# Performance work log

Hardware: AMD Instinct MI355X
Metric: run time of the kernel (lower is better)

## Reference

```python
import jax, jax.numpy as jnp
import numpy as np
from jax import lax

N_LAYER = 4
D_MODEL = 1024
D_INNER = 2048   # expand=2
D_STATE = 16
DT_RANK = 64     # ceil(d_model/16)
D_CONV = 4
BATCH = 2
SEQ = 2048
EPS = 1e-5


def setup_inputs() -> dict:
    key = jax.random.key(0)
    ks = jax.random.split(key, 8)
    rn = lambda k, shape, s=0.02: jax.random.normal(k, shape, dtype=jnp.float32) * s
    # S4D-real init for A_log, as in mamba_ssm
    A_init = jnp.tile(jnp.arange(1, D_STATE + 1, dtype=jnp.float32)[None, None, :],
                      (N_LAYER, D_INNER, 1))
    return {
        "hidden_states": jax.random.normal(ks[0], (BATCH, SEQ, D_MODEL), dtype=jnp.float32),
        "norm_w": jnp.ones((N_LAYER, D_MODEL), jnp.float32),
        "norm_b": jnp.zeros((N_LAYER, D_MODEL), jnp.float32),
        "in_proj_w": rn(ks[1], (N_LAYER, 2 * D_INNER, D_MODEL)),
        "conv_w": rn(ks[2], (N_LAYER, D_INNER, D_CONV), 0.1),
        "conv_b": jnp.zeros((N_LAYER, D_INNER), jnp.float32),
        "x_proj_w": rn(ks[3], (N_LAYER, DT_RANK + 2 * D_STATE, D_INNER)),
        "dt_proj_w": rn(ks[4], (N_LAYER, D_INNER, DT_RANK), 0.1),
        "dt_proj_b": rn(ks[5], (N_LAYER, D_INNER), 0.1),
        "A_log": jnp.log(A_init),
        "D": jnp.ones((N_LAYER, D_INNER), jnp.float32),
        "out_proj_w": rn(ks[6], (N_LAYER, D_MODEL, D_INNER)),
        "final_norm_w": jnp.ones((D_MODEL,), jnp.float32),
        "final_norm_b": jnp.zeros((D_MODEL,), jnp.float32),
    }


def _layernorm(x, w, b):
    mu = jnp.mean(x, axis=-1, keepdims=True)
    var = jnp.mean(jnp.square(x - mu), axis=-1, keepdims=True)
    return (x - mu) * lax.rsqrt(var + EPS) * w + b


def _mamba_block(h, in_w, conv_w, conv_b, x_w, dt_w, dt_b, A_log, Dp, out_w):
    B, L, _ = h.shape
    xz = jnp.einsum('bld,ed->ble', h, in_w)               # [B,L,2*d_inner]
    x, z = jnp.split(xz, 2, axis=-1)
    # depthwise causal conv1d (kernel D_CONV), truncated to L
    xp = jnp.pad(x, ((0, 0), (D_CONV - 1, 0), (0, 0)))
    x = sum(xp[:, k:k + L, :] * conv_w[:, k] for k in range(D_CONV)) + conv_b
    x = jax.nn.silu(x)
    x_dbl = jnp.einsum('bld,ed->ble', x, x_w)             # [B,L,dt_rank+2*d_state]
    dt, Bm, Cm = jnp.split(x_dbl, [DT_RANK, DT_RANK + D_STATE], axis=-1)
    delta = jax.nn.softplus(jnp.einsum('blr,dr->bld', dt, dt_w) + dt_b)  # [B,L,d_inner]
    A = -jnp.exp(A_log)                                   # [d_inner, d_state]

    def step(state, xs):
        d_t, B_t, C_t, u_t = xs                           # [B,di],[B,ds],[B,ds],[B,di]
        dA = jnp.exp(d_t[..., None] * A)                  # [B,di,ds]
        state = dA * state + (d_t * u_t)[..., None] * B_t[:, None, :]
        y_t = jnp.einsum('bds,bs->bd', state, C_t)
        return state, y_t

    xs = (jnp.swapaxes(delta, 0, 1), jnp.swapaxes(Bm, 0, 1),
          jnp.swapaxes(Cm, 0, 1), jnp.swapaxes(x, 0, 1))
    init = jnp.zeros((B, D_INNER, D_STATE), dtype=h.dtype)
    _, ys = lax.scan(step, init, xs)                      # ys: [L,B,di]
    y = jnp.swapaxes(ys, 0, 1) + x * Dp
    y = y * jax.nn.silu(z)
    return jnp.einsum('bld,ed->ble', y, out_w)            # [B,L,d_model]


def reference(hidden_states, norm_w, norm_b, in_proj_w, conv_w, conv_b,
              x_proj_w, dt_proj_w, dt_proj_b, A_log, D, out_proj_w,
              final_norm_w, final_norm_b):
    residual = None
    for i in range(N_LAYER):
        residual = hidden_states + residual if residual is not None else hidden_states
        h = _layernorm(residual, norm_w[i], norm_b[i])
        hidden_states = _mamba_block(h, in_proj_w[i], conv_w[i], conv_b[i],
                                     x_proj_w[i], dt_proj_w[i], dt_proj_b[i],
                                     A_log[i], D[i], out_proj_w[i])
    residual = hidden_states + residual
    return _layernorm(residual, final_norm_w, final_norm_b)
```

## Files before the change

kernel.cpp:

```cpp
#include <hip/hip_runtime.h>
#include <math.h>

#define N_LAYERS 4
#define DMODEL 1024
#define DINNER 2048
#define DSTATE 16
#define DTRANK 64
#define DCONV 4
#define NBATCH 2
#define LSEQ 2048
#define LNEPS 1e-5f
#define ROWS (NBATCH * LSEQ)
#define CLEN 16
#define NCHUNK (LSEQ / CLEN)
#define XP 128
#define KSLICE 512
#define NSLICE (DINNER / KSLICE)

typedef __attribute__((ext_vector_type(8))) short bf16x8;
typedef __attribute__((ext_vector_type(8))) unsigned short ushort8;
typedef __attribute__((ext_vector_type(4))) float f32x4;

__device__ __forceinline__ unsigned short f2bf(float f) {
  unsigned int u = __float_as_uint(f);
  return (unsigned short)((u + 0x7FFFu + ((u >> 16) & 1u)) >> 16);
}
__device__ __forceinline__ float bf2f(unsigned short h) {
  return __uint_as_float(((unsigned int)h) << 16);
}

__device__ __forceinline__ void gload16(const unsigned short* g, unsigned short* l) {
  __builtin_amdgcn_global_load_lds(
      (const __attribute__((address_space(1))) unsigned int*)g,
      (__attribute__((address_space(3))) unsigned int*)l, 16, 0, 0);
}

__device__ __forceinline__ float softplus_f(float x) {
  float e = __expf(-fabsf(x));
  return fmaxf(x, 0.f) + __logf(1.f + e);
}

__global__ __launch_bounds__(256) void cvt_f2bf(const float* __restrict__ src,
                                                unsigned short* __restrict__ dst, int n4) {
  int i = blockIdx.x * 256 + threadIdx.x;
  if (i >= n4) return;
  float4 v = ((const float4*)src)[i];
  ushort4 o;
  o.x = f2bf(v.x); o.y = f2bf(v.y); o.z = f2bf(v.z); o.w = f2bf(v.w);
  ((ushort4*)dst)[i] = o;
}

__global__ __launch_bounds__(256) void cvt_xpw(const float* __restrict__ src,
                                               unsigned short* __restrict__ dst) {
  int i = blockIdx.x * 256 + threadIdx.x;
  int col4 = i & 511;
  int row = (i >> 9) & 127;
  int layer = i >> 16;
  float4 v = make_float4(0.f, 0.f, 0.f, 0.f);
  if (row < 96) v = ((const float4*)(src + ((size_t)layer * 96 + row) * 2048))[col4];
  ushort4 o;
  o.x = f2bf(v.x); o.y = f2bf(v.y); o.z = f2bf(v.z); o.w = f2bf(v.w);
  ((ushort4*)(dst + ((size_t)layer * 128 + row) * 2048))[col4] = o;
}

template<bool OBF>
__global__ __launch_bounds__(256) void ln_kernel(
    const float* __restrict__ src, float* __restrict__ res_copy,
    const float* __restrict__ w, const float* __restrict__ b, void* out) {
  int row = blockIdx.x;
  int t = threadIdx.x;
  const float4* srow = (const float4*)(src + (size_t)row * DMODEL);
  float4 v = srow[t];
  if (res_copy) ((float4*)(res_copy + (size_t)row * DMODEL))[t] = v;
  float s = v.x + v.y + v.z + v.w;
  float sq = v.x * v.x + v.y * v.y + v.z * v.z + v.w * v.w;
  #pragma unroll
  for (int o = 32; o >= 1; o >>= 1) {
    s += __shfl_xor(s, o);
    sq += __shfl_xor(sq, o);
  }
  __shared__ float ss[4], ssq[4];
  int wid = t >> 6, lane = t & 63;
  if (lane == 0) { ss[wid] = s; ssq[wid] = sq; }
  __syncthreads();
  s = ss[0] + ss[1] + ss[2] + ss[3];
  sq = ssq[0] + ssq[1] + ssq[2] + ssq[3];
  float mu = s * (1.f / DMODEL);
  float var = sq * (1.f / DMODEL) - mu * mu;
  float rs = rsqrtf(var + LNEPS);
  float4 wv = ((const float4*)w)[t];
  float4 bv = ((const float4*)b)[t];
  float4 o4;
  o4.x = (v.x - mu) * rs * wv.x + bv.x;
  o4.y = (v.y - mu) * rs * wv.y + bv.y;
  o4.z = (v.z - mu) * rs * wv.z + bv.z;
  o4.w = (v.w - mu) * rs * wv.w + bv.w;
  if (OBF) {
    ushort4 ob;
    ob.x = f2bf(o4.x); ob.y = f2bf(o4.y); ob.z = f2bf(o4.z); ob.w = f2bf(o4.w);
    ((ushort4*)((unsigned short*)out + (size_t)row * DMODEL))[t] = ob;
  } else {
    ((float4*)((float*)out + (size_t)row * DMODEL))[t] = o4;
  }
}

template<int ACT, bool BIAS, bool ADD, bool WF32, bool WBF>
__global__ __launch_bounds__(512) void gemm256(
    const unsigned short* __restrict__ A, int lda,
    const unsigned short* __restrict__ W, int ldw,
    float* __restrict__ C, int ldc, int K,
    const float* __restrict__ bias,
    const float* __restrict__ addsrc,
    unsigned short* __restrict__ Cb) {
  __shared__ unsigned short lds[2][2][256][64];
  const int t = threadIdx.x;
  const int lane = t & 63;
  const int wave = t >> 6;
  const int wr = wave >> 2;
  const int wc = wave & 3;
  const int m0 = blockIdx.y * 256, n0 = blockIdx.x * 256;

  const int srow = t >> 3;
  const int sslot = t & 7;
  const int frow = lane & 15;
  const int hi = lane >> 4;

  f32x4 acc[8][4];
  #pragma unroll
  for (int m = 0; m < 8; m++)
    #pragma unroll
    for (int n = 0; n < 4; n++) acc[m][n] = (f32x4){0.f, 0.f, 0.f, 0.f};

  const int NT = K / 64;

  auto stage = [&](int buf, int kt) {
    const int scol = (sslot << 3) + kt * 64;
    #pragma unroll
    for (int r = 0; r < 4; ++r) {
      int row = srow + (r << 6);
      gload16(A + (size_t)(m0 + row) * lda + scol, &lds[buf][0][row][sslot << 3]);
    }
    #pragma unroll
    for (int r = 0; r < 4; ++r) {
      int row = srow + (r << 6);
      gload16(W + (size_t)(n0 + row) * ldw + scol, &lds[buf][1][row][sslot << 3]);
    }
  };

  auto compute = [&](int buf) {
    #pragma unroll
    for (int ks = 0; ks < 2; ++ks) {
      bf16x8 a[8], b[4];
      #pragma unroll
      for (int m = 0; m < 8; ++m) {
        int row = wr * 128 + m * 16 + frow;
        a[m] = *(const bf16x8*)&lds[buf][0][row][(ks * 4 + hi) << 3];
      }
      #pragma unroll
      for (int n = 0; n < 4; ++n) {
        int row = wc * 64 + n * 16 + frow;
        b[n] = *(const bf16x8*)&lds[buf][1][row][(ks * 4 + hi) << 3];
      }
      __builtin_amdgcn_s_setprio(1);
      #pragma unroll
      for (int m = 0; m < 8; ++m)
        #pragma unroll
        for (int n = 0; n < 4; ++n)
          acc[m][n] = __builtin_amdgcn_mfma_f32_16x16x32_bf16(a[m], b[n], acc[m][n], 0, 0, 0);
      __builtin_amdgcn_s_setprio(0);
    }
  };

  stage(0, 0);
  if (NT > 1) stage(1, 1);
  for (int kt = 0; kt < NT - 1; ++kt) {
    asm volatile("s_waitcnt vmcnt(8)" ::: "memory");
    __builtin_amdgcn_s_barrier();
    asm volatile("" ::: "memory");
    compute(kt & 1);
    __builtin_amdgcn_s_barrier();
    asm volatile("" ::: "memory");
    if (kt + 2 < NT) stage(kt & 1, kt + 2);
  }
  asm volatile("s_waitcnt vmcnt(0)" ::: "memory");
  __builtin_amdgcn_s_barrier();
  asm volatile("" ::: "memory");
  compute((NT - 1) & 1);

  #pragma unroll
  for (int m = 0; m < 8; ++m) {
    int rbase = m0 + wr * 128 + m * 16 + hi * 4;
    #pragma unroll
    for (int n = 0; n < 4; ++n) {
      int ccol = n0 + wc * 64 + n * 16 + frow;
      #pragma unroll
      for (int j = 0; j < 4; ++j) {
        int crow = rbase + j;
        float v = acc[m][n][j];
        if (BIAS) v += bias[ccol];
        if (ACT == 1) v = softplus_f(v);
        if (ADD) v += addsrc[(size_t)crow * ldc + ccol];
        if (WF32) C[(size_t)crow * ldc + ccol] = v;
        if (WBF) Cb[(size_t)crow * ldc + ccol] = f2bf(v);
      }
    }
  }
}

template<int ACT, bool BIAS, bool ADD, bool WF32, bool WBF, bool PARTIAL>
__global__ __launch_bounds__(256) void gemm_bf16(
    const unsigned short* __restrict__ A, int lda,
    const unsigned short* __restrict__ W, int ldw,
    float* __restrict__ C, int ldc, int K,
    const float* __restrict__ bias,
    const float* __restrict__ addsrc,
    unsigned short* __restrict__ Cb) {
  __shared__ unsigned short As[2][128][32];
  __shared__ unsigned short Ws[2][128][32];
  int t = threadIdx.x;
  int lane = t & 63, wave = t >> 6;
  int wr = wave >> 1, wc = wave & 1;
  int m0 = blockIdx.y * 128, n0 = blockIdx.x * 128;

  int kbase = 0;
  if (PARTIAL) {
    kbase = blockIdx.z * K;
    C += (size_t)blockIdx.z * (size_t)gridDim.y * 128 * ldc;
  }

  int r0 = t >> 2;
  int kk8 = (t & 3) << 3;
  const unsigned short* Ag = A + (size_t)(m0 + r0) * lda + kbase + kk8;
  const unsigned short* Wg = W + (size_t)(n0 + r0) * ldw + kbase + kk8;
  const size_t Astep = (size_t)64 * lda;
  const size_t Wstep = (size_t)64 * ldw;

  f32x4 zero = {0.f, 0.f, 0.f, 0.f};
  f32x4 acc[4][4];
  #pragma unroll
  for (int m = 0; m < 4; m++)
    #pragma unroll
    for (int n = 0; n < 4; n++) acc[m][n] = zero;

  int frow = lane & 15;
  int fk = (lane >> 4) << 3;

  auto stage = [&](int buf, int kt) {
    const unsigned short* ag = Ag + kt * 32;
    const unsigned short* wg = Wg + kt * 32;
    unsigned short* la = &As[buf][r0][kk8];
    unsigned short* lw = &Ws[buf][r0][kk8];
    gload16(ag, la);
    gload16(ag + Astep, la + 64 * 32);
    gload16(wg, lw);
    gload16(wg + Wstep, lw + 64 * 32);
  };
  auto compute = [&](int buf) {
    bf16x8 af[4], bw[4];
    #pragma unroll
    for (int m = 0; m < 4; m++)
      af[m] = *(const bf16x8*)&As[buf][wr * 64 + m * 16 + frow][fk];
    #pragma unroll
    for (int n = 0; n < 4; n++)
      bw[n] = *(const bf16x8*)&Ws[buf][wc * 64 + n * 16 + frow][fk];
    #pragma unroll
    for (int m = 0; m < 4; m++)
      #pragma unroll
      for (int n = 0; n < 4; n++)
        acc[m][n] = __builtin_amdgcn_mfma_f32_16x16x32_bf16(af[m], bw[n], acc[m][n], 0, 0, 0);
  };

  const int NT = K / 32;
  stage(0, 0);
  __syncthreads();
  int cur = 0;
  for (int kt = 0; kt < NT - 1; ++kt) {
    stage(cur ^ 1, kt + 1);
    compute(cur);
    __syncthreads();
    cur ^= 1;
  }
  compute(cur);

  #pragma unroll
  for (int m = 0; m < 4; m++) {
    int rbase = m0 + wr * 64 + m * 16 + ((lane >> 4) << 2);
    #pragma unroll
    for (int n = 0; n < 4; n++) {
      int ccol = n0 + wc * 64 + n * 16 + (lane & 15);
      #pragma unroll
      for (int j = 0; j < 4; j++) {
        int crow = rbase + j;
        float v = acc[m][n][j];
        if (BIAS) v += bias[ccol];
        if (ACT == 1) v = softplus_f(v);
        if (ADD) v += addsrc[(size_t)crow * ldc + ccol];
        if (WF32 || PARTIAL) C[(size_t)crow * ldc + ccol] = v;
        if (WBF) Cb[(size_t)crow * ldc + ccol] = f2bf(v);
      }
    }
  }
}

__global__ __launch_bounds__(256) void combine_xdbl(
    const float* __restrict__ part, float* __restrict__ xdbl,
    unsigned short* __restrict__ xdbl_bf) {
  int i = blockIdx.x * 256 + threadIdx.x;
  const size_t slab = (size_t)ROWS * XP / 4;
  const float4* p = (const float4*)part;
  float4 a = p[i], b = p[i + slab], c = p[i + 2 * slab], d = p[i + 3 * slab];
  float4 s;
  s.x = a.x + b.x + c.x + d.x;
  s.y = a.y + b.y + c.y + d.y;
  s.z = a.z + b.z + c.z + d.z;
  s.w = a.w + b.w + c.w + d.w;
  ((float4*)xdbl)[i] = s;
  ushort4 o;
  o.x = f2bf(s.x); o.y = f2bf(s.y); o.z = f2bf(s.z); o.w = f2bf(s.w);
  ((ushort4*)xdbl_bf)[i] = o;
}

__global__ __launch_bounds__(256) void conv_silu_kernel(
    const unsigned short* __restrict__ xz, const float* __restrict__ cw,
    const float* __restrict__ cb, unsigned short* __restrict__ xbf) {
  int tid = blockIdx.x * 256 + threadIdx.x;
  int dv = tid & (DINNER / 8 - 1);
  int rg = tid >> 8;
  int l0 = (rg & (LSEQ / 4 - 1)) * 4;
  int row0 = rg * 4;
  int d = dv * 8;

  float4 wq[8];
  #pragma unroll
  for (int j = 0; j < 8; j++) wq[j] = ((const float4*)(cw + (size_t)d * DCONV))[j];
  float4 b0 = ((const float4*)(cb + d))[0];
  float4 b1 = ((const float4*)(cb + d))[1];
  const float bias[8] = {b0.x, b0.y, b0.z, b0.w, b1.x, b1.y, b1.z, b1.w};

  ushort8 xin[7];
  #pragma unroll
  for (int r = 0; r < 7; r++) {
    int l = l0 - 3 + r;
    if (l >= 0)
      xin[r] = *(const ushort8*)(xz + (size_t)(row0 - 3 + r) * (2 * DINNER) + d);
    else
      xin[r] = (ushort8){0, 0, 0, 0, 0, 0, 0, 0};
  }

  #pragma unroll
  for (int o = 0; o < 4; o++) {
    ushort8 ob;
    #pragma unroll
    for (int j = 0; j < 8; j++) {
      const float* wj = (const float*)&wq[j];
      float acc = bias[j];
      #pragma unroll
      for (int k = 0; k < DCONV; k++)
        acc = fmaf(bf2f(xin[o + k][j]), wj[k], acc);
      float s = acc / (1.f + __expf(-acc));
      ob[j] = f2bf(s);
    }
    *(ushort8*)(xbf + (size_t)(row0 + o) * DINNER + d) = ob;
  }
}

__global__ __launch_bounds__(256) void scan_p1(
    const float* __restrict__ delta, const unsigned short* __restrict__ u,
    const float* __restrict__ xdbl, const float* __restrict__ A_log,
    float* __restrict__ aprodbuf, float* __restrict__ statebuf) {
  int tid = blockIdx.x * 256 + threadIdx.x;
  int t = threadIdx.x;
  int d = tid & (DINNER - 1);
  int chunk = (tid >> 11) & (NCHUNK - 1);
  int b = tid >> 18;
  int l0 = chunk * CLEN;

  __shared__ float bl[CLEN][16];
  {
    const float4* src4 = (const float4*)(xdbl + ((size_t)b * LSEQ + l0) * XP);
    if (t < CLEN * 4) {
      int li = t >> 2, qi = t & 3;
      ((float4*)&bl[li][0])[qi] = src4[li * (XP / 4) + 16 + qi];
    }
  }
  __syncthreads();

  float A[DSTATE], st[DSTATE], ap[DSTATE];
  const float4* Ar = (const float4*)(A_log + d * DSTATE);
  #pragma unroll
  for (int q = 0; q < 4; q++) {
    float4 av = Ar[q];
    A[4 * q] = -__expf(av.x); A[4 * q + 1] = -__expf(av.y);
    A[4 * q + 2] = -__expf(av.z); A[4 * q + 3] = -__expf(av.w);
  }
  #pragma unroll
  for (int s = 0; s < DSTATE; s++) { st[s] = 0.f; ap[s] = 1.f; }

  const float* dptr = delta + ((size_t)b * LSEQ + l0) * DINNER + d;
  const unsigned short* uptr = u + ((size_t)b * LSEQ + l0) * DINNER + d;
  float dt_n = dptr[0];
  float uu_n = bf2f(uptr[0]);
  #pragma unroll
  for (int l = 0; l < CLEN; l++) {
    float dt = dt_n, uu = uu_n;
    if (l + 1 < CLEN) {
      dt_n = dptr[(size_t)(l + 1) * DINNER];
      uu_n = bf2f(uptr[(size_t)(l + 1) * DINNER]);
    }
    float du = dt * uu;
    #pragma unroll
    for (int q = 0; q < 4; q++) {
      float4 B4 = *(const float4*)&bl[l][q * 4];
      const float Bj[4] = {B4.x, B4.y, B4.z, B4.w};
      #pragma unroll
      for (int j = 0; j < 4; j++) {
        int s = 4 * q + j;
        float dA = __expf(dt * A[s]);
        st[s] = fmaf(dA, st[s], du * Bj[j]);
        ap[s] *= dA;
      }
    }
  }
  float4* apo = (float4*)(aprodbuf + (size_t)tid * DSTATE);
  float4* sto = (float4*)(statebuf + (size_t)tid * DSTATE);
  #pragma unroll
  for (int q = 0; q < 4; q++) {
    apo[q] = make_float4(ap[4 * q], ap[4 * q + 1], ap[4 * q + 2], ap[4 * q + 3]);
    sto[q] = make_float4(st[4 * q], st[4 * q + 1], st[4 * q + 2], st[4 * q + 3]);
  }
}

__global__ __launch_bounds__(256) void scan_p2(
    float* apc, const float* __restrict__ statebuf) {
  int tid = blockIdx.x * 256 + threadIdx.x;
  int ds = tid & (DINNER * DSTATE - 1);
  int b = tid >> 15;
  float carry = 0.f;
  size_t base = (size_t)b * NCHUNK * DINNER * DSTATE + ds;
  const size_t cs = DINNER * DSTATE;
  for (int c = 0; c < NCHUNK; c += 4) {
    size_t i0 = base + (size_t)c * cs;
    float a0 = apc[i0], a1 = apc[i0 + cs], a2 = apc[i0 + 2 * cs], a3 = apc[i0 + 3 * cs];
    float s0 = statebuf[i0], s1 = statebuf[i0 + cs];
    float s2 = statebuf[i0 + 2 * cs], s3 = statebuf[i0 + 3 * cs];
    apc[i0] = carry;          carry = fmaf(a0, carry, s0);
    apc[i0 + cs] = carry;     carry = fmaf(a1, carry, s1);
    apc[i0 + 2 * cs] = carry; carry = fmaf(a2, carry, s2);
    apc[i0 + 3 * cs] = carry; carry = fmaf(a3, carry, s3);
  }
}

__global__ __launch_bounds__(256) void scan_p3(
    const float* __restrict__ delta, const unsigned short* __restrict__ u,
    const float* __restrict__ xdbl, const unsigned short* __restrict__ xzbf,
    const float* __restrict__ A_log, const float* __restrict__ Dp,
    const float* __restrict__ carryin, unsigned short* __restrict__ ybf) {
  int tid = blockIdx.x * 256 + threadIdx.x;
  int t = threadIdx.x;
  int d = tid & (DINNER - 1);
  int chunk = (tid >> 11) & (NCHUNK - 1);
  int b = tid >> 18;
  int l0 = chunk * CLEN;

  __shared__ float bc[CLEN][32];
  {
    const float4* src4 = (const float4*)(xdbl + ((size_t)b * LSEQ + l0) * XP);
    if (t < CLEN * 8) {
      int li = t >> 3, qi = t & 7;
      ((float4*)&bc[li][0])[qi] = src4[li * (XP / 4) + 16 + qi];
    }
  }
  __syncthreads();

  float A[DSTATE], st[DSTATE];
  const float4* ci = (const float4*)(carryin + (size_t)tid * DSTATE);
  #pragma unroll
  for (int q = 0; q < 4; q++) {
    float4 cv = ci[q];
    st[4 * q] = cv.x; st[4 * q + 1] = cv.y; st[4 * q + 2] = cv.z; st[4 * q + 3] = cv.w;
  }
  const float4* Ar = (const float4*)(A_log + d * DSTATE);
  #pragma unroll
  for (int q = 0; q < 4; q++) {
    float4 av = Ar[q];
    A[4 * q] = -__expf(av.x); A[4 * q + 1] = -__expf(av.y);
    A[4 * q + 2] = -__expf(av.z); A[4 * q + 3] = -__expf(av.w);
  }
  float Dval = Dp[d];

  const float* dptr = delta + ((size_t)b * LSEQ + l0) * DINNER + d;
  const unsigned short* uptr = u + ((size_t)b * LSEQ + l0) * DINNER + d;
  const unsigned short* zptr = xzbf + ((size_t)b * LSEQ + l0) * (2 * DINNER) + DINNER + d;
  unsigned short* yptr = ybf + ((size_t)b * LSEQ + l0) * DINNER + d;

  float dt_n = dptr[0];
  float uu_n = bf2f(uptr[0]);
  float zz_n = bf2f(zptr[0]);
  #pragma unroll
  for (int l = 0; l < CLEN; l++) {
    float dt = dt_n, uu = uu_n, zz = zz_n;
    if (l + 1 < CLEN) {
      dt_n = dptr[(size_t)(l + 1) * DINNER];
      uu_n = bf2f(uptr[(size_t)(l + 1) * DINNER]);
      zz_n = bf2f(zptr[(size_t)(l + 1) * (2 * DINNER)]);
    }
    float du = dt * uu;
    #pragma unroll
    for (int q = 0; q < 4; q++) {
      float4 B4 = *(const float4*)&bc[l][q * 4];
      const float Bj[4] = {B4.x, B4.y, B4.z, B4.w};
      #pragma unroll
      for (int j = 0; j < 4; j++) {
        int s = 4 * q + j;
        float dA = __expf(dt * A[s]);
        st[s] = fmaf(dA, st[s], du * Bj[j]);
      }
    }
    float acc = 0.f;
    #pragma unroll
    for (int q = 0; q < 4; q++) {
      float4 C4 = *(const float4*)&bc[l][16 + q * 4];
      const float Cj[4] = {C4.x, C4.y, C4.z, C4.w};
      #pragma unroll
      for (int j = 0; j < 4; j++) acc = fmaf(st[4 * q + j], Cj[j], acc);
    }
    float yv = (acc + uu * Dval) * (zz / (1.f + __expf(-zz)));
    yptr[(size_t)l * DINNER] = f2bf(yv);
  }
}

extern "C" void kernel_launch(void* const* d_in, const int* in_sizes, int n_in,
                              void* d_out, int out_size, void* d_ws, size_t ws_size,
                              hipStream_t stream) {
  const float* hidden    = (const float*)d_in[0];
  const float* norm_w    = (const float*)d_in[1];
  const float* norm_b    = (const float*)d_in[2];
  const float* in_proj_w = (const float*)d_in[3];
  const float* conv_w    = (const float*)d_in[4];
  const float* conv_b    = (const float*)d_in[5];
  const float* x_proj_w  = (const float*)d_in[6];
  const float* dt_proj_w = (const float*)d_in[7];
  const float* dt_proj_b = (const float*)d_in[8];
  const float* A_log     = (const float*)d_in[9];
  const float* Dp        = (const float*)d_in[10];
  const float* out_proj_w= (const float*)d_in[11];
  const float* fnw       = (const float*)d_in[12];
  const float* fnb       = (const float*)d_in[13];
  float* out = (float*)d_out;

  const size_t CARRYSZ = (size_t)NBATCH * NCHUNK * DINNER * DSTATE;

  float* residual = (float*)d_ws;
  float* delta    = residual + (size_t)ROWS * DMODEL;
  float* aprod    = delta + (size_t)ROWS * DINNER;
  float* statebuf = aprod + CARRYSZ;
  float* xdbl     = statebuf + CARRYSZ;
  float* fend     = xdbl + (size_t)ROWS * XP;

  unsigned short* xz_bf   = (unsigned short*)fend;
  unsigned short* xbuf_bf = xz_bf + (size_t)ROWS * 2 * DINNER;
  unsigned short* xdbl_bf = xbuf_bf + (size_t)ROWS * DINNER;
  unsigned short* xpw_bf  = xdbl_bf + (size_t)ROWS * XP;
  unsigned short* dtw_bf  = xpw_bf + (size_t)N_LAYERS * XP * DINNER;
  unsigned short* ipw_bf  = dtw_bf + (size_t)N_LAYERS * DINNER * DTRANK;
  unsigned short* opw_bf  = ipw_bf + (size_t)2 * DINNER * DMODEL;

  unsigned short* h_bf    = (unsigned short*)statebuf;
  unsigned short* ybuf_bf = (unsigned short*)statebuf;
  float*          carryin = aprod;
  float*          xpart   = delta;

  cvt_xpw<<<N_LAYERS * XP * DINNER / 4 / 256, 256, 0, stream>>>(x_proj_w, xpw_bf);
  {
    int n4 = N_LAYERS * DINNER * DTRANK / 4;
    cvt_f2bf<<<n4 / 256, 256, 0, stream>>>(dt_proj_w, dtw_bf, n4);
  }

  for (int i = 0; i < N_LAYERS; i++) {
    {
      int n4 = 2 * DINNER * DMODEL / 4;
      cvt_f2bf<<<n4 / 256, 256, 0, stream>>>(
          in_proj_w + (size_t)i * 2 * DINNER * DMODEL, ipw_bf, n4);
      n4 = DMODEL * DINNER / 4;
      cvt_f2bf<<<n4 / 256, 256, 0, stream>>>(
          out_proj_w + (size_t)i * DMODEL * DINNER, opw_bf, n4);
    }
    ln_kernel<true><<<ROWS, 256, 0, stream>>>(
        i == 0 ? hidden : residual, i == 0 ? residual : nullptr,
        norm_w + (size_t)i * DMODEL, norm_b + (size_t)i * DMODEL, h_bf);
    {
      dim3 g(2 * DINNER / 256, ROWS / 256);
      gemm256<0, false, false, false, true><<<g, 512, 0, stream>>>(
          h_bf, DMODEL, ipw_bf, DMODEL, nullptr, 2 * DINNER, DMODEL,
          nullptr, nullptr, xz_bf);
    }
    conv_silu_kernel<<<ROWS / 4 * DINNER / 8 / 256, 256, 0, stream>>>(
        xz_bf, conv_w + (size_t)i * DINNER * DCONV, conv_b + (size_t)i * DINNER,
        xbuf_bf);
    {
      dim3 g(1, ROWS / 128, NSLICE);
      gemm_bf16<0, false, false, true, false, true><<<g, 256, 0, stream>>>(
          xbuf_bf, DINNER, xpw_bf + (size_t)i * XP * DINNER, DINNER,
          xpart, XP, KSLICE, nullptr, nullptr, nullptr);
      combine_xdbl<<<ROWS * XP / 4 / 256, 256, 0, stream>>>(xpart, xdbl, xdbl_bf);
    }
    {
      dim3 g(DINNER / 128, ROWS / 128);
      gemm_bf16<1, true, false, true, false, false><<<g, 256, 0, stream>>>(
          xdbl_bf, XP, dtw_bf + (size_t)i * DINNER * DTRANK, DTRANK,
          delta, DINNER, DTRANK, dt_proj_b + (size_t)i * DINNER,
          nullptr, nullptr);
    }
    scan_p1<<<NBATCH * NCHUNK * DINNER / 256, 256, 0, stream>>>(
        delta, xbuf_bf, xdbl, A_log + (size_t)i * DINNER * DSTATE, aprod, statebuf);
    scan_p2<<<NBATCH * DINNER * DSTATE / 256, 256, 0, stream>>>(aprod, statebuf);
    scan_p3<<<NBATCH * NCHUNK * DINNER / 256, 256, 0, stream>>>(
        delta, xbuf_bf, xdbl, xz_bf, A_log + (size_t)i * DINNER * DSTATE,
        Dp + (size_t)i * DINNER, carryin, ybuf_bf);
    {
      dim3 g(DMODEL / 128, ROWS / 128);
      gemm_bf16<0, false, true, true, false, false><<<g, 256, 0, stream>>>(
          ybuf_bf, DINNER, opw_bf, DINNER,
          residual, DMODEL, DINNER, nullptr, residual, nullptr);
    }
  }
  ln_kernel<false><<<ROWS, 256, 0, stream>>>(residual, nullptr, fnw, fnb, out);
}
```

Before: 958.4 us.

## Double scan chunk length and pack inter-chunk carries as bf16

Chunk length for the chunked selective scan goes from 16 to 32, which halves the number of chunks and the size of the per-chunk carry buffers. The per-chunk decay product and state are packed as two bf16 values in one 32-bit word, and the propagated carry-in is also stored as bf16. This cuts the traffic through the carry buffers, and the scan inner loops are only partially unrolled to limit register pressure. The cost is less precision in the inter-chunk state, longer serial work per thread, and fewer threads in flight. The workspace layout is reorganized because the carry buffers no longer alias h/y.

New measurement: 918.4 us. 4.2% less time.

```diff
diff --git a/kernel.cpp b/kernel.cpp
--- a/kernel.cpp
+++ b/kernel.cpp
@@ -11,7 +11,7 @@
 #define LSEQ 2048
 #define LNEPS 1e-5f
 #define ROWS (NBATCH * LSEQ)
-#define CLEN 16
+#define CLEN 32
 #define NCHUNK (LSEQ / CLEN)
 #define XP 128
 #define KSLICE 512
@@ -20,6 +20,7 @@
 typedef __attribute__((ext_vector_type(8))) short bf16x8;
 typedef __attribute__((ext_vector_type(8))) unsigned short ushort8;
 typedef __attribute__((ext_vector_type(4))) float f32x4;
+typedef __attribute__((ext_vector_type(4))) unsigned int uint4v;
 
 __device__ __forceinline__ unsigned short f2bf(float f) {
   unsigned int u = __float_as_uint(f);
@@ -367,12 +368,12 @@
 __global__ __launch_bounds__(256) void scan_p1(
     const float* __restrict__ delta, const unsigned short* __restrict__ u,
     const float* __restrict__ xdbl, const float* __restrict__ A_log,
-    float* __restrict__ aprodbuf, float* __restrict__ statebuf) {
+    unsigned int* __restrict__ carrybuf) {
   int tid = blockIdx.x * 256 + threadIdx.x;
   int t = threadIdx.x;
   int d = tid & (DINNER - 1);
   int chunk = (tid >> 11) & (NCHUNK - 1);
-  int b = tid >> 18;
+  int b = tid >> 17;
   int l0 = chunk * CLEN;
 
   __shared__ float bl[CLEN][16];
@@ -400,7 +401,7 @@
   const unsigned short* uptr = u + ((size_t)b * LSEQ + l0) * DINNER + d;
   float dt_n = dptr[0];
   float uu_n = bf2f(uptr[0]);
-  #pragma unroll
+  #pragma unroll 4
   for (int l = 0; l < CLEN; l++) {
     float dt = dt_n, uu = uu_n;
     if (l + 1 < CLEN) {
@@ -421,17 +422,19 @@
       }
     }
   }
-  float4* apo = (float4*)(aprodbuf + (size_t)tid * DSTATE);
-  float4* sto = (float4*)(statebuf + (size_t)tid * DSTATE);
+  uint4v* co = (uint4v*)(carrybuf + (size_t)tid * DSTATE);
   #pragma unroll
   for (int q = 0; q < 4; q++) {
-    apo[q] = make_float4(ap[4 * q], ap[4 * q + 1], ap[4 * q + 2], ap[4 * q + 3]);
-    sto[q] = make_float4(st[4 * q], st[4 * q + 1], st[4 * q + 2], st[4 * q + 3]);
+    uint4v v;
+    #pragma unroll
+    for (int j = 0; j < 4; j++)
+      v[j] = ((unsigned int)f2bf(ap[4 * q + j]) << 16) | f2bf(st[4 * q + j]);
+    co[q] = v;
   }
 }
 
 __global__ __launch_bounds__(256) void scan_p2(
-    float* apc, const float* __restrict__ statebuf) {
+    const unsigned int* __restrict__ cbuf, unsigned short* __restrict__ carryin) {
   int tid = blockIdx.x * 256 + threadIdx.x;
   int ds = tid & (DINNER * DSTATE - 1);
   int b = tid >> 15;
@@ -440,13 +443,16 @@
   const size_t cs = DINNER * DSTATE;
   for (int c = 0; c < NCHUNK; c += 4) {
     size_t i0 = base + (size_t)c * cs;
-    float a0 = apc[i0], a1 = apc[i0 + cs], a2 = apc[i0 + 2 * cs], a3 = apc[i0 + 3 * cs];
-    float s0 = statebuf[i0], s1 = statebuf[i0 + cs];
-    float s2 = statebuf[i0 + 2 * cs], s3 = statebuf[i0 + 3 * cs];
-    apc[i0] = carry;          carry = fmaf(a0, carry, s0);
-    apc[i0 + cs] = carry;     carry = fmaf(a1, carry, s1);
-    apc[i0 + 2 * cs] = carry; carry = fmaf(a2, carry, s2);
-    apc[i0 + 3 * cs] = carry; carry = fmaf(a3, carry, s3);
+    unsigned int v0 = cbuf[i0], v1 = cbuf[i0 + cs];
+    unsigned int v2 = cbuf[i0 + 2 * cs], v3 = cbuf[i0 + 3 * cs];
+    carryin[i0] = f2bf(carry);
+    carry = fmaf(bf2f(v0 >> 16), carry, bf2f(v0 & 0xFFFFu));
+    carryin[i0 + cs] = f2bf(carry);
+    carry = fmaf(bf2f(v1 >> 16), carry, bf2f(v1 & 0xFFFFu));
+    carryin[i0 + 2 * cs] = f2bf(carry);
+    carry = fmaf(bf2f(v2 >> 16), carry, bf2f(v2 & 0xFFFFu));
+    carryin[i0 + 3 * cs] = f2bf(carry);
+    carry = fmaf(bf2f(v3 >> 16), carry, bf2f(v3 & 0xFFFFu));
   }
 }
 
@@ -454,30 +460,28 @@
     const float* __restrict__ delta, const unsigned short* __restrict__ u,
     const float* __restrict__ xdbl, const unsigned short* __restrict__ xzbf,
     const float* __restrict__ A_log, const float* __restrict__ Dp,
-    const float* __restrict__ carryin, unsigned short* __restrict__ ybf) {
+    const unsigned short* __restrict__ carryin, unsigned short* __restrict__ ybf) {
   int tid = blockIdx.x * 256 + threadIdx.x;
   int t = threadIdx.x;
   int d = tid & (DINNER - 1);
   int chunk = (tid >> 11) & (NCHUNK - 1);
-  int b = tid >> 18;
+  int b = tid >> 17;
   int l0 = chunk * CLEN;
 
   __shared__ float bc[CLEN][32];
   {
     const float4* src4 = (const float4*)(xdbl + ((size_t)b * LSEQ + l0) * XP);
-    if (t < CLEN * 8) {
-      int li = t >> 3, qi = t & 7;
-      ((float4*)&bc[li][0])[qi] = src4[li * (XP / 4) + 16 + qi];
-    }
+    int li = t >> 3, qi = t & 7;
+    ((float4*)&bc[li][0])[qi] = src4[li * (XP / 4) + 16 + qi];
   }
   __syncthreads();
 
   float A[DSTATE], st[DSTATE];
-  const float4* ci = (const float4*)(carryin + (size_t)tid * DSTATE);
-  #pragma unroll
-  for (int q = 0; q < 4; q++) {
-    float4 cv = ci[q];
-    st[4 * q] = cv.x; st[4 * q + 1] = cv.y; st[4 * q + 2] = cv.z; st[4 * q + 3] = cv.w;
+  {
+    const ushort8* ci8 = (const ushort8*)(carryin + (size_t)tid * DSTATE);
+    ushort8 c0 = ci8[0], c1 = ci8[1];
+    #pragma unroll
+    for (int j = 0; j < 8; j++) { st[j] = bf2f(c0[j]); st[8 + j] = bf2f(c1[j]); }
   }
   const float4* Ar = (const float4*)(A_log + d * DSTATE);
   #pragma unroll
@@ -496,7 +500,7 @@
   float dt_n = dptr[0];
   float uu_n = bf2f(uptr[0]);
   float zz_n = bf2f(zptr[0]);
-  #pragma unroll
+  #pragma unroll 4
   for (int l = 0; l < CLEN; l++) {
     float dt = dt_n, uu = uu_n, zz = zz_n;
     if (l + 1 < CLEN) {
@@ -552,23 +556,23 @@
 
   float* residual = (float*)d_ws;
   float* delta    = residual + (size_t)ROWS * DMODEL;
-  float* aprod    = delta + (size_t)ROWS * DINNER;
-  float* statebuf = aprod + CARRYSZ;
-  float* xdbl     = statebuf + CARRYSZ;
+  float* xdbl     = delta + (size_t)ROWS * DINNER;
   float* fend     = xdbl + (size_t)ROWS * XP;
 
   unsigned short* xz_bf   = (unsigned short*)fend;
   unsigned short* xbuf_bf = xz_bf + (size_t)ROWS * 2 * DINNER;
-  unsigned short* xdbl_bf = xbuf_bf + (size_t)ROWS * DINNER;
+  unsigned short* h_bf    = xbuf_bf + (size_t)ROWS * DINNER;
+  unsigned short* ybuf_bf = h_bf + (size_t)ROWS * DMODEL;
+  unsigned short* xdbl_bf = ybuf_bf + (size_t)ROWS * DINNER;
   unsigned short* xpw_bf  = xdbl_bf + (size_t)ROWS * XP;
   unsigned short* dtw_bf  = xpw_bf + (size_t)N_LAYERS * XP * DINNER;
   unsigned short* ipw_bf  = dtw_bf + (size_t)N_LAYERS * DINNER * DTRANK;
   unsigned short* opw_bf  = ipw_bf + (size_t)2 * DINNER * DMODEL;
-
-  unsigned short* h_bf    = (unsigned short*)statebuf;
-  unsigned short* ybuf_bf = (unsigned short*)statebuf;
-  float*          carryin = aprod;
-  float*          xpart   = delta;
+  unsigned short* usend   = opw_bf + (size_t)DMODEL * DINNER;
+
+  unsigned int*   carrybuf = (unsigned int*)usend;
+  unsigned short* carryin  = (unsigned short*)(carrybuf + CARRYSZ);
+  float*          xpart    = delta;
 
   cvt_xpw<<<N_LAYERS * XP * DINNER / 4 / 256, 256, 0, stream>>>(x_proj_w, xpw_bf);
   {
@@ -612,8 +616,8 @@
           nullptr, nullptr);
     }
     scan_p1<<<NBATCH * NCHUNK * DINNER / 256, 256, 0, stream>>>(
-        delta, xbuf_bf, xdbl, A_log + (size_t)i * DINNER * DSTATE, aprod, statebuf);
-    scan_p2<<<NBATCH * DINNER * DSTATE / 256, 256, 0, stream>>>(aprod, statebuf);
+        delta, xbuf_bf, xdbl, A_log + (size_t)i * DINNER * DSTATE, carrybuf);
+    scan_p2<<<NBATCH * DINNER * DSTATE / 256, 256, 0, stream>>>(carrybuf, carryin);
     scan_p3<<<NBATCH * NCHUNK * DINNER / 256, 256, 0, stream>>>(
         delta, xbuf_bf, xdbl, xz_bf, A_log + (size_t)i * DINNER * DSTATE,
         Dp + (size_t)i * DINNER, carryin, ybuf_bf);
```
